# Optimization experiments

Hardware: AMD Instinct MI355X
Metric: run time of the kernel (lower is better)

The kernel has to match this reference:

```python
import jax, jax.numpy as jnp
import numpy as np

N_NEURONS = 4096
N_EDGES = 131072
N_LAYERS = 2
VOCAB = 8192
B, T = 8, 128
DECAY = 0.99


def setup_inputs() -> dict:
    key = jax.random.key(0)
    ks = jax.random.split(key, 8)
    idx = jax.random.randint(ks[0], (B, T), 0, VOCAB)
    src = jax.random.randint(ks[1], (N_EDGES,), 0, N_NEURONS)
    dst = jax.random.randint(ks[2], (N_EDGES,), 0, N_NEURONS)
    Wemb = jax.random.normal(ks[3], (VOCAB, N_NEURONS), dtype=jnp.float32) * 0.02
    Gx = jax.random.normal(ks[4], (N_EDGES,), dtype=jnp.float32) * 0.02
    Gy = jax.random.normal(ks[5], (N_EDGES,), dtype=jnp.float32) * 0.02
    Gs = jnp.ones((N_EDGES,), dtype=jnp.float32)
    W_out = jax.random.normal(ks[6], (VOCAB, N_NEURONS), dtype=jnp.float32) * 0.02
    b_out = jnp.zeros((VOCAB,), dtype=jnp.float32)
    return {"idx": idx, "src": src, "dst": dst, "Wemb": Wemb, "Gx": Gx,
            "Gy": Gy, "Gs": Gs, "W_out": W_out, "b_out": b_out}


def reference(idx, src, dst, Wemb, Gx, Gy, Gs, W_out, b_out):
    # X: [B, T, n] token embeddings
    X = Wemb[idx]
    sigma0 = jnp.zeros((src.shape[0],), dtype=Wemb.dtype)
    y0 = X[:, 0, :]  # initial y_t = embedding of first token
    Xt = jnp.transpose(X, (1, 0, 2))  # [T, B, n] for scan over time

    def step(carry, x_t):
        y_t, sigma = carry
        for _ in range(N_LAYERS):
            # A[:, d] += x_t[:, s] * sigma  (gather-mul-scatter over edges)
            A = jnp.zeros_like(x_t).at[:, dst].add(x_t[:, src] * sigma)
            # Hebbian plasticity update on edge state sigma
            hebbian = (y_t[:, src] * x_t[:, dst]).mean(0)
            sigma = (sigma + hebbian * Gs) * DECAY
            y_t = jnp.zeros_like(x_t).at[:, dst].add(jax.nn.relu(A[:, src]) * Gy)
            x_t = jax.nn.relu(jnp.zeros_like(x_t).at[:, dst].add(y_t[:, src] * Gx))
        return (y_t, sigma), x_t

    (_, sigma_final), xs = jax.lax.scan(step, (y0, sigma0), Xt)  # xs: [T, B, n]
    logits = jnp.einsum('tbn,vn->btv', xs, W_out) + b_out  # [B, T, vocab]
    return logits, sigma_final
```

## Files before the change

kernel.cpp:

```cpp
#include <hip/hip_runtime.h>
#include <cstdint>
#include <cstddef>

#define NN   4096
#define NE   131072
#define NBAT 8
#define NT   128
#define NV   8192
#define NK   4096
#define NM   1024
#define DECAYF 0.99f
#define COOP_BLOCKS 256
#define COOP_THREADS 1024
#define NBARRIERS (NT * 5)

typedef short bf16x8 __attribute__((ext_vector_type(8)));
typedef float f32x4 __attribute__((ext_vector_type(4)));
typedef unsigned short u16x8 __attribute__((ext_vector_type(8)));

__device__ __forceinline__ unsigned short f2bf(float f) {
  unsigned int u = __builtin_bit_cast(unsigned int, f);
  u = u + 0x7fffu + ((u >> 16) & 1u);
  return (unsigned short)(u >> 16);
}

__device__ __forceinline__ float cload(const float* p) {
  return __hip_atomic_load(p, __ATOMIC_RELAXED, __HIP_MEMORY_SCOPE_AGENT);
}
__device__ __forceinline__ void cstore(float* p, float v) {
  __hip_atomic_store(p, v, __ATOMIC_RELAXED, __HIP_MEMORY_SCOPE_AGENT);
}
__device__ __forceinline__ int cloadi(const int* p) {
  return __hip_atomic_load(p, __ATOMIC_RELAXED, __HIP_MEMORY_SCOPE_AGENT);
}
__device__ __forceinline__ void cstorei(int* p, int v) {
  __hip_atomic_store(p, v, __ATOMIC_RELAXED, __HIP_MEMORY_SCOPE_AGENT);
}

__global__ void k_hist(const int* __restrict__ dst, int* __restrict__ cnt) {
  int e = blockIdx.x * 256 + threadIdx.x;
  if (e < NE) atomicAdd(&cnt[dst[e]], 1);
}

__global__ void k_scan(const int* __restrict__ cnt, int* __restrict__ row_ptr,
                       int* __restrict__ cursor) {
  __shared__ int lds[256];
  int tid = threadIdx.x;
  int base = tid * 16;
  int loc[16];
  int s = 0;
  #pragma unroll
  for (int i = 0; i < 16; ++i) { loc[i] = s; s += cnt[base + i]; }
  lds[tid] = s;
  __syncthreads();
  for (int off = 1; off < 256; off <<= 1) {
    int v = lds[tid];
    int a = (tid >= off) ? lds[tid - off] : 0;
    __syncthreads();
    lds[tid] = v + a;
    __syncthreads();
  }
  int myoff = (tid == 0) ? 0 : lds[tid - 1];
  #pragma unroll
  for (int i = 0; i < 16; ++i) {
    int rp = myoff + loc[i];
    row_ptr[base + i] = rp;
    cursor[base + i] = rp;
  }
  if (tid == 255) row_ptr[NN] = lds[255];
}

__global__ void k_build(const int* __restrict__ src, const int* __restrict__ dst,
                        const float* __restrict__ Gx, const float* __restrict__ Gy,
                        const float* __restrict__ Gs, int* __restrict__ cursor,
                        int* __restrict__ src_s, int* __restrict__ orig_s,
                        float* __restrict__ Gx_s, float* __restrict__ Gy_s,
                        float* __restrict__ Gs_s) {
  int e = blockIdx.x * 256 + threadIdx.x;
  if (e >= NE) return;
  int d = dst[e];
  int pos = atomicAdd(&cursor[d], 1);
  src_s[pos] = src[e];
  orig_s[pos] = e;
  Gx_s[pos] = Gx[e];
  Gy_s[pos] = Gy[e];
  Gs_s[pos] = Gs[e];
}

__global__ void k_gatherX(const int* __restrict__ idx, const float* __restrict__ Wemb,
                          float* __restrict__ Xbuf, float* __restrict__ ybuf) {
  __shared__ float tile[256 * 9];
  int t = blockIdx.x >> 4;
  int nc = (blockIdx.x & 15) << 8;
  int tid = threadIdx.x;
  #pragma unroll
  for (int bb = 0; bb < 8; ++bb) {
    int row = idx[bb * NT + t];
    tile[tid * 9 + bb] = Wemb[(size_t)row * NN + nc + tid];
  }
  __syncthreads();
  float* dp = Xbuf + (size_t)t * (NN * NBAT) + (size_t)nc * NBAT;
  #pragma unroll
  for (int kk = 0; kk < 8; ++kk) dp[tid * 8 + kk] = tile[tid * 9 + kk];
  if (t == 0) {
    float* yp = ybuf + (size_t)nc * NBAT;
    #pragma unroll
    for (int kk = 0; kk < 8; ++kk) yp[tid * 8 + kk] = tile[tid * 9 + kk];
  }
}

__global__ void k_convW(const float* __restrict__ W, unsigned short* __restrict__ Wbf) {
  size_t base = ((size_t)blockIdx.x * 256 + threadIdx.x) * 8;
  float4 a = *(const float4*)(W + base);
  float4 b = *(const float4*)(W + base + 4);
  u16x8 hv;
  hv[0] = f2bf(a.x); hv[1] = f2bf(a.y); hv[2] = f2bf(a.z); hv[3] = f2bf(a.w);
  hv[4] = f2bf(b.x); hv[5] = f2bf(b.y); hv[6] = f2bf(b.z); hv[7] = f2bf(b.w);
  *(u16x8*)(Wbf + base) = hv;
}

__device__ __forceinline__ void gridbar(int* bar, int& gen) {
  __syncthreads();
  if (threadIdx.x == 0) {
    cstorei(&bar[blockIdx.x], gen + 1);
    while (cloadi(&bar[320]) <= gen) __builtin_amdgcn_s_sleep(1);
  }
  ++gen;
  __syncthreads();
}

__global__ __launch_bounds__(COOP_THREADS, 8) void k_loop(
    const int* __restrict__ row_ptr, const int* __restrict__ src_s,
    const float* __restrict__ Gx_s, const float* __restrict__ Gy_s,
    const float* __restrict__ Gs_s, float* __restrict__ sigma_s,
    const float* __restrict__ Xbuf, float* __restrict__ ybuf,
    float* __restrict__ xbuf, float* __restrict__ Abuf,
    unsigned short* __restrict__ Abf, int* bar,
    const int* __restrict__ orig_s, float* __restrict__ sig_out) {
  if (blockIdx.x == COOP_BLOCKS) {
    if (threadIdx.x < 64) {
      const int lane = threadIdx.x;
      for (int g = 1; g <= NBARRIERS; ++g) {
        for (;;) {
          int v0 = cloadi(&bar[lane * 4 + 0]);
          int v1 = cloadi(&bar[lane * 4 + 1]);
          int v2 = cloadi(&bar[lane * 4 + 2]);
          int v3 = cloadi(&bar[lane * 4 + 3]);
          int m = min(min(v0, v1), min(v2, v3));
          #pragma unroll
          for (int d = 1; d < 64; d <<= 1) m = min(m, __shfl_xor(m, d));
          if (m >= g) break;
        }
        if (lane == 0) cstorei(&bar[320], g);
      }
    }
    return;
  }

  const int tid = threadIdx.x;
  const int g = blockIdx.x * COOP_THREADS + tid;
  const int b = g & 7;
  const int h = (g >> 3) & 7;
  const int n = g >> 6;
  const int rs = row_ptr[n];
  const int re = row_ptr[n + 1];
  const int nb8 = (n << 3) | b;
  int gen = 0;

  for (int t = 0; t < NT; ++t) {
    const float* xp = Xbuf + (size_t)t * (NN * NBAT);
    #pragma unroll
    for (int layer = 0; layer < 2; ++layer) {
      {
        float xn = (layer == 0) ? xp[nb8] : cload(&xbuf[nb8]);
        float acc = 0.f;
        for (int j = rs + h; j < re; j += 32) {
          int jj[4], sv[4];
          float sg[4], gs[4], xv[4], yv[4];
          bool act[4];
          #pragma unroll
          for (int u = 0; u < 4; ++u) {
            int jc = j + (u << 3);
            act[u] = jc < re;
            jj[u] = act[u] ? jc : j;
          }
          #pragma unroll
          for (int u = 0; u < 4; ++u) sv[u] = src_s[jj[u]];
          #pragma unroll
          for (int u = 0; u < 4; ++u) {
            float sgu = sigma_s[jj[u]];
            float gsu = Gs_s[jj[u]];
            sg[u] = act[u] ? sgu : 0.f;
            gs[u] = act[u] ? gsu : 0.f;
          }
          #pragma unroll
          for (int u = 0; u < 4; ++u) {
            int sb = (sv[u] << 3) | b;
            xv[u] = (layer == 0) ? xp[sb] : cload(&xbuf[sb]);
            yv[u] = cload(&ybuf[sb]);
          }
          #pragma unroll
          for (int u = 0; u < 4; ++u) {
            acc = fmaf(xv[u], sg[u], acc);
            float pv = yv[u] * xn;
            pv += __shfl_xor(pv, 1);
            pv += __shfl_xor(pv, 2);
            pv += __shfl_xor(pv, 4);
            if (b == 0 && act[u])
              sigma_s[jj[u]] = (sg[u] + pv * 0.125f * gs[u]) * DECAYF;
          }
        }
        acc += __shfl_xor(acc, 8);
        acc += __shfl_xor(acc, 16);
        acc += __shfl_xor(acc, 32);
        if (h == 0) cstore(&Abuf[nb8], acc);
      }
      gridbar(bar, gen);
      {
        float acc = 0.f;
        for (int j = rs + h; j < re; j += 32) {
          int jj[4], sv[4];
          float gy[4], av[4];
          bool act[4];
          #pragma unroll
          for (int u = 0; u < 4; ++u) {
            int jc = j + (u << 3);
            act[u] = jc < re;
            jj[u] = act[u] ? jc : j;
          }
          #pragma unroll
          for (int u = 0; u < 4; ++u) sv[u] = src_s[jj[u]];
          #pragma unroll
          for (int u = 0; u < 4; ++u) {
            float gyu = Gy_s[jj[u]];
            gy[u] = act[u] ? gyu : 0.f;
          }
          #pragma unroll
          for (int u = 0; u < 4; ++u) av[u] = cload(&Abuf[(sv[u] << 3) | b]);
          #pragma unroll
          for (int u = 0; u < 4; ++u) acc = fmaf(fmaxf(av[u], 0.f), gy[u], acc);
        }
        acc += __shfl_xor(acc, 8);
        acc += __shfl_xor(acc, 16);
        acc += __shfl_xor(acc, 32);
        if (h == 0) cstore(&ybuf[nb8], acc);
      }
      gridbar(bar, gen);
      {
        float acc = 0.f;
        for (int j = rs + h; j < re; j += 32) {
          int jj[4], sv[4];
          float gx[4], yv[4];
          bool act[4];
          #pragma unroll
          for (int u = 0; u < 4; ++u) {
            int jc = j + (u << 3);
            act[u] = jc < re;
            jj[u] = act[u] ? jc : j;
          }
          #pragma unroll
          for (int u = 0; u < 4; ++u) sv[u] = src_s[jj[u]];
          #pragma unroll
          for (int u = 0; u < 4; ++u) {
            float gxu = Gx_s[jj[u]];
            gx[u] = act[u] ? gxu : 0.f;
          }
          #pragma unroll
          for (int u = 0; u < 4; ++u) yv[u] = cload(&ybuf[(sv[u] << 3) | b]);
          #pragma unroll
          for (int u = 0; u < 4; ++u) acc = fmaf(yv[u], gx[u], acc);
        }
        acc += __shfl_xor(acc, 8);
        acc += __shfl_xor(acc, 16);
        acc += __shfl_xor(acc, 32);
        if (layer == 0) {
          if (h == 0) cstore(&xbuf[nb8], fmaxf(acc, 0.f));
        } else if (h == 0) {
          Abf[(size_t)((b << 7) | t) * NK + n] = f2bf(fmaxf(acc, 0.f));
        }
      }
      if (layer == 0) {
        gridbar(bar, gen);
        xp = xbuf;
      }
    }
  }
  __syncthreads();
  int jlo = row_ptr[blockIdx.x * 16];
  int jhi = row_ptr[blockIdx.x * 16 + 16];
  for (int j = jlo + tid; j < jhi; j += COOP_THREADS) sig_out[orig_s[j]] = sigma_s[j];
}

__global__ __launch_bounds__(256) void k_gemm(const unsigned short* __restrict__ A,
                                              const unsigned short* __restrict__ Bw,
                                              const float* __restrict__ bias,
                                              float* __restrict__ C) {
  __shared__ __align__(16) unsigned short As[128 * 32];
  __shared__ __align__(16) unsigned short Bs[128 * 32];
  const int m0 = blockIdx.y * 128;
  const int v0 = blockIdx.x * 128;
  const int wave = threadIdx.x >> 6;
  const int lane = threadIdx.x & 63;
  const int wm = wave >> 1;
  const int wv = wave & 1;
  f32x4 acc[4][4] = {};

  const int srow = lane >> 2;
  const int skc = (lane & 3) * 8;

  for (int k0 = 0; k0 < NK; k0 += 32) {
    #pragma unroll
    for (int c = 0; c < 2; ++c) {
      int chunk = wave * 2 + c;
      int row = chunk * 16 + srow;
      __builtin_amdgcn_global_load_lds(
          (const __attribute__((address_space(1))) void*)(A + (size_t)(m0 + row) * NK + k0 + skc),
          (__attribute__((address_space(3))) void*)(As + chunk * 512), 16, 0, 0);
      __builtin_amdgcn_global_load_lds(
          (const __attribute__((address_space(1))) void*)(Bw + (size_t)(v0 + row) * NK + k0 + skc),
          (__attribute__((address_space(3))) void*)(Bs + chunk * 512), 16, 0, 0);
    }
    __syncthreads();
    bf16x8 af[4], bq[4];
    #pragma unroll
    for (int mi = 0; mi < 4; ++mi)
      af[mi] = *(const bf16x8*)(As + ((wm * 64 + mi * 16 + (lane & 15)) * 32 + (lane >> 4) * 8));
    #pragma unroll
    for (int ni = 0; ni < 4; ++ni)
      bq[ni] = *(const bf16x8*)(Bs + ((wv * 64 + ni * 16 + (lane & 15)) * 32 + (lane >> 4) * 8));
    #pragma unroll
    for (int mi = 0; mi < 4; ++mi)
      #pragma unroll
      for (int ni = 0; ni < 4; ++ni)
        acc[mi][ni] = __builtin_amdgcn_mfma_f32_16x16x32_bf16(af[mi], bq[ni], acc[mi][ni], 0, 0, 0);
    __syncthreads();
  }

  #pragma unroll
  for (int mi = 0; mi < 4; ++mi) {
    int mrow = m0 + wm * 64 + mi * 16 + ((lane >> 4) << 2);
    #pragma unroll
    for (int ni = 0; ni < 4; ++ni) {
      int vcol = v0 + wv * 64 + ni * 16 + (lane & 15);
      float bs = bias[vcol];
      f32x4 a = acc[mi][ni];
      #pragma unroll
      for (int r = 0; r < 4; ++r) C[(size_t)(mrow + r) * NV + vcol] = a[r] + bs;
    }
  }
}

extern "C" void kernel_launch(void* const* d_in, const int* in_sizes, int n_in,
                              void* d_out, int out_size, void* d_ws, size_t ws_size,
                              hipStream_t stream) {
  (void)in_sizes; (void)n_in; (void)out_size;
  const int*   idx  = (const int*)d_in[0];
  const int*   src  = (const int*)d_in[1];
  const int*   dst  = (const int*)d_in[2];
  const float* Wemb = (const float*)d_in[3];
  const float* Gx   = (const float*)d_in[4];
  const float* Gy   = (const float*)d_in[5];
  const float* Gs   = (const float*)d_in[6];
  const float* Wout = (const float*)d_in[7];
  const float* bout = (const float*)d_in[8];
  float* out = (float*)d_out;
  float* sig_out = out + (size_t)NM * NV;

  char* p = (char*)d_ws;
  int*   bar     = (int*)p;
  int*   cnt     = (int*)(p + 2048);
  float* sigma_s = (float*)(p + 2048 + 16384);
  size_t off = 2048 + 16384 + (size_t)NE * 4;
  const size_t msz = off;
  int*   row_ptr = (int*)(p + off); off += 16640;
  int*   cursor  = (int*)(p + off); off += 16384;
  int*   src_s   = (int*)(p + off); off += (size_t)NE * 4;
  int*   orig_s  = (int*)(p + off); off += (size_t)NE * 4;
  float* Gx_s    = (float*)(p + off); off += (size_t)NE * 4;
  float* Gy_s    = (float*)(p + off); off += (size_t)NE * 4;
  float* Gs_s    = (float*)(p + off); off += (size_t)NE * 4;
  float* ybuf    = (float*)(p + off); off += (size_t)NN * NBAT * 4;
  float* xbuf    = (float*)(p + off); off += (size_t)NN * NBAT * 4;
  float* Abuf    = (float*)(p + off); off += (size_t)NN * NBAT * 4;
  float* Xbuf    = (float*)(p + off); off += (size_t)NT * NN * NBAT * 4;
  unsigned short* Abf = (unsigned short*)(p + off); off += (size_t)NM * NK * 2;
  unsigned short* Wbf = (unsigned short*)(p + off); off += (size_t)NV * NK * 2;
  if (ws_size < off) return;

  hipMemsetAsync(d_ws, 0, msz, stream);
  k_hist<<<NE / 256, 256, 0, stream>>>(dst, cnt);
  k_scan<<<1, 256, 0, stream>>>(cnt, row_ptr, cursor);
  k_build<<<NE / 256, 256, 0, stream>>>(src, dst, Gx, Gy, Gs, cursor,
                                        src_s, orig_s, Gx_s, Gy_s, Gs_s);
  k_gatherX<<<NT * 16, 256, 0, stream>>>(idx, Wemb, Xbuf, ybuf);
  k_convW<<<(NV * NK) / (256 * 8), 256, 0, stream>>>(Wout, Wbf);
  k_loop<<<COOP_BLOCKS + 1, COOP_THREADS, 0, stream>>>(row_ptr, src_s, Gx_s, Gy_s, Gs_s,
      sigma_s, Xbuf, ybuf, xbuf, Abuf, Abf, bar, orig_s, sig_out);
  k_gemm<<<dim3(NV / 128, NM / 128), 256, 0, stream>>>(Abf, Wbf, bout, out);
}
```

Before: 3.414 ms.

## Keep per-edge sigma and source indices in registers, interleave x/y buffers

Each thread now caches its first 8 edges' source indices and sigma values in registers for the whole time loop, with a sentinel padded slot so that loads need no masking. Edges beyond 64 per destination fall back to a memory loop. x and y states are interleaved so layer-1 reads both with one 64-bit load. The grid barrier now releases through a per-block padded flag instead of one shared word, to cut contention on that word. This adds register pressure and a tail path for high in-degree nodes.

```diff
diff --git a/kernel.cpp b/kernel.cpp
--- a/kernel.cpp
+++ b/kernel.cpp
@@ -27,6 +27,11 @@
 __device__ __forceinline__ float cload(const float* p) {
   return __hip_atomic_load(p, __ATOMIC_RELAXED, __HIP_MEMORY_SCOPE_AGENT);
 }
+__device__ __forceinline__ float2 cload2(const float* p) {
+  unsigned long long v = __hip_atomic_load((const unsigned long long*)p,
+                                           __ATOMIC_RELAXED, __HIP_MEMORY_SCOPE_AGENT);
+  return __builtin_bit_cast(float2, v);
+}
 __device__ __forceinline__ void cstore(float* p, float v) {
   __hip_atomic_store(p, v, __ATOMIC_RELAXED, __HIP_MEMORY_SCOPE_AGENT);
 }
@@ -78,6 +83,10 @@
                         float* __restrict__ Gs_s) {
   int e = blockIdx.x * 256 + threadIdx.x;
   if (e >= NE) return;
+  if (e == 0) {
+    src_s[NE] = 0;
+    Gx_s[NE] = 0.f; Gy_s[NE] = 0.f; Gs_s[NE] = 0.f;
+  }
   int d = dst[e];
   int pos = atomicAdd(&cursor[d], 1);
   src_s[pos] = src[e];
@@ -88,7 +97,7 @@
 }
 
 __global__ void k_gatherX(const int* __restrict__ idx, const float* __restrict__ Wemb,
-                          float* __restrict__ Xbuf, float* __restrict__ ybuf) {
+                          float* __restrict__ Xbuf, float* __restrict__ xybuf) {
   __shared__ float tile[256 * 9];
   int t = blockIdx.x >> 4;
   int nc = (blockIdx.x & 15) << 8;
@@ -103,9 +112,9 @@
   #pragma unroll
   for (int kk = 0; kk < 8; ++kk) dp[tid * 8 + kk] = tile[tid * 9 + kk];
   if (t == 0) {
-    float* yp = ybuf + (size_t)nc * NBAT;
-    #pragma unroll
-    for (int kk = 0; kk < 8; ++kk) yp[tid * 8 + kk] = tile[tid * 9 + kk];
+    float* yp = xybuf + (size_t)nc * NBAT * 2;
+    #pragma unroll
+    for (int kk = 0; kk < 8; ++kk) yp[((tid * 8 + kk) << 1) + 1] = tile[tid * 9 + kk];
   }
 }
 
@@ -119,11 +128,11 @@
   *(u16x8*)(Wbf + base) = hv;
 }
 
-__device__ __forceinline__ void gridbar(int* bar, int& gen) {
+__device__ __forceinline__ void gridbar(int* bar, int* rel, int& gen) {
   __syncthreads();
   if (threadIdx.x == 0) {
     cstorei(&bar[blockIdx.x], gen + 1);
-    while (cloadi(&bar[320]) <= gen) __builtin_amdgcn_s_sleep(1);
+    while (cloadi(&rel[blockIdx.x << 4]) <= gen) __builtin_amdgcn_s_sleep(1);
   }
   ++gen;
   __syncthreads();
@@ -133,25 +142,26 @@
     const int* __restrict__ row_ptr, const int* __restrict__ src_s,
     const float* __restrict__ Gx_s, const float* __restrict__ Gy_s,
     const float* __restrict__ Gs_s, float* __restrict__ sigma_s,
-    const float* __restrict__ Xbuf, float* __restrict__ ybuf,
-    float* __restrict__ xbuf, float* __restrict__ Abuf,
-    unsigned short* __restrict__ Abf, int* bar,
+    const float* __restrict__ Xbuf, float* __restrict__ xybuf,
+    float* __restrict__ Abuf, unsigned short* __restrict__ Abf,
+    int* bar, int* rel,
     const int* __restrict__ orig_s, float* __restrict__ sig_out) {
   if (blockIdx.x == COOP_BLOCKS) {
     if (threadIdx.x < 64) {
       const int lane = threadIdx.x;
       for (int g = 1; g <= NBARRIERS; ++g) {
         for (;;) {
-          int v0 = cloadi(&bar[lane * 4 + 0]);
-          int v1 = cloadi(&bar[lane * 4 + 1]);
-          int v2 = cloadi(&bar[lane * 4 + 2]);
-          int v3 = cloadi(&bar[lane * 4 + 3]);
+          int v0 = cloadi(&bar[lane]);
+          int v1 = cloadi(&bar[lane + 64]);
+          int v2 = cloadi(&bar[lane + 128]);
+          int v3 = cloadi(&bar[lane + 192]);
           int m = min(min(v0, v1), min(v2, v3));
           #pragma unroll
           for (int d = 1; d < 64; d <<= 1) m = min(m, __shfl_xor(m, d));
           if (m >= g) break;
         }
-        if (lane == 0) cstorei(&bar[320], g);
+        #pragma unroll
+        for (int k = 0; k < 4; ++k) cstorei(&rel[(lane + k * 64) << 4], g);
       }
     }
     return;
@@ -164,50 +174,63 @@
   const int n = g >> 6;
   const int rs = row_ptr[n];
   const int re = row_ptr[n + 1];
+  const int rh = rs + h;
   const int nb8 = (n << 3) | b;
+  const int nb16 = nb8 << 1;
   int gen = 0;
+
+  int   r_sb[8];
+  float r_sg[8];
+  #pragma unroll
+  for (int s = 0; s < 8; ++s) {
+    int jc = rh + ((s >> 2) << 5) + ((s & 3) << 3);
+    int j = (jc < re) ? jc : NE;
+    r_sb[s] = (src_s[j] << 3) | b;
+    r_sg[s] = 0.f;
+  }
+  const bool tail = (re - rs) > 64;
 
   for (int t = 0; t < NT; ++t) {
     const float* xp = Xbuf + (size_t)t * (NN * NBAT);
     #pragma unroll
     for (int layer = 0; layer < 2; ++layer) {
       {
-        float xn = (layer == 0) ? xp[nb8] : cload(&xbuf[nb8]);
+        float xn = (layer == 0) ? xp[nb8] : cload(&xybuf[nb16]);
+        float xv[8], yv[8];
+        #pragma unroll
+        for (int s = 0; s < 8; ++s) {
+          if (layer == 0) {
+            xv[s] = xp[r_sb[s]];
+            yv[s] = cload(&xybuf[(r_sb[s] << 1) + 1]);
+          } else {
+            float2 p2 = cload2(&xybuf[r_sb[s] << 1]);
+            xv[s] = p2.x; yv[s] = p2.y;
+          }
+        }
         float acc = 0.f;
-        for (int j = rs + h; j < re; j += 32) {
-          int jj[4], sv[4];
-          float sg[4], gs[4], xv[4], yv[4];
-          bool act[4];
-          #pragma unroll
-          for (int u = 0; u < 4; ++u) {
-            int jc = j + (u << 3);
-            act[u] = jc < re;
-            jj[u] = act[u] ? jc : j;
-          }
-          #pragma unroll
-          for (int u = 0; u < 4; ++u) sv[u] = src_s[jj[u]];
-          #pragma unroll
-          for (int u = 0; u < 4; ++u) {
-            float sgu = sigma_s[jj[u]];
-            float gsu = Gs_s[jj[u]];
-            sg[u] = act[u] ? sgu : 0.f;
-            gs[u] = act[u] ? gsu : 0.f;
-          }
-          #pragma unroll
-          for (int u = 0; u < 4; ++u) {
-            int sb = (sv[u] << 3) | b;
-            xv[u] = (layer == 0) ? xp[sb] : cload(&xbuf[sb]);
-            yv[u] = cload(&ybuf[sb]);
-          }
-          #pragma unroll
-          for (int u = 0; u < 4; ++u) {
-            acc = fmaf(xv[u], sg[u], acc);
-            float pv = yv[u] * xn;
-            pv += __shfl_xor(pv, 1);
-            pv += __shfl_xor(pv, 2);
-            pv += __shfl_xor(pv, 4);
-            if (b == 0 && act[u])
-              sigma_s[jj[u]] = (sg[u] + pv * 0.125f * gs[u]) * DECAYF;
+        #pragma unroll
+        for (int s = 0; s < 8; ++s) {
+          acc = fmaf(xv[s], r_sg[s], acc);
+          float pv = yv[s] * xn;
+          pv += __shfl_xor(pv, 1);
+          pv += __shfl_xor(pv, 2);
+          pv += __shfl_xor(pv, 4);
+          int jc = rh + ((s >> 2) << 5) + ((s & 3) << 3);
+          int j = (jc < re) ? jc : NE;
+          r_sg[s] = (r_sg[s] + pv * 0.125f * Gs_s[j]) * DECAYF;
+        }
+        if (tail) {
+          for (int j = rs + 64 + h; j < re; j += 8) {
+            int sb2 = ((src_s[j] << 3) | b) << 1;
+            float xvr = (layer == 0) ? xp[sb2 >> 1] : cload(&xybuf[sb2]);
+            float yvr = cload(&xybuf[sb2 + 1]);
+            float sgr = sigma_s[j];
+            acc = fmaf(xvr, sgr, acc);
+            float pvr = yvr * xn;
+            pvr += __shfl_xor(pvr, 1);
+            pvr += __shfl_xor(pvr, 2);
+            pvr += __shfl_xor(pvr, 4);
+            if (b == 0) sigma_s[j] = (sgr + pvr * 0.125f * Gs_s[j]) * DECAYF;
           }
         }
         acc += __shfl_xor(acc, 8);
@@ -215,80 +238,62 @@
         acc += __shfl_xor(acc, 32);
         if (h == 0) cstore(&Abuf[nb8], acc);
       }
-      gridbar(bar, gen);
+      gridbar(bar, rel, gen);
       {
+        float av[8];
+        #pragma unroll
+        for (int s = 0; s < 8; ++s) av[s] = cload(&Abuf[r_sb[s]]);
         float acc = 0.f;
-        for (int j = rs + h; j < re; j += 32) {
-          int jj[4], sv[4];
-          float gy[4], av[4];
-          bool act[4];
-          #pragma unroll
-          for (int u = 0; u < 4; ++u) {
-            int jc = j + (u << 3);
-            act[u] = jc < re;
-            jj[u] = act[u] ? jc : j;
-          }
-          #pragma unroll
-          for (int u = 0; u < 4; ++u) sv[u] = src_s[jj[u]];
-          #pragma unroll
-          for (int u = 0; u < 4; ++u) {
-            float gyu = Gy_s[jj[u]];
-            gy[u] = act[u] ? gyu : 0.f;
-          }
-          #pragma unroll
-          for (int u = 0; u < 4; ++u) av[u] = cload(&Abuf[(sv[u] << 3) | b]);
-          #pragma unroll
-          for (int u = 0; u < 4; ++u) acc = fmaf(fmaxf(av[u], 0.f), gy[u], acc);
-        }
+        #pragma unroll
+        for (int s = 0; s < 8; ++s) {
+          int jc = rh + ((s >> 2) << 5) + ((s & 3) << 3);
+          int j = (jc < re) ? jc : NE;
+          acc = fmaf(fmaxf(av[s], 0.f), Gy_s[j], acc);
+        }
+        if (tail)
+          for (int j = rs + 64 + h; j < re; j += 8)
+            acc = fmaf(fmaxf(cload(&Abuf[(src_s[j] << 3) | b]), 0.f), Gy_s[j], acc);
         acc += __shfl_xor(acc, 8);
         acc += __shfl_xor(acc, 16);
         acc += __shfl_xor(acc, 32);
-        if (h == 0) cstore(&ybuf[nb8], acc);
+        if (h == 0) cstore(&xybuf[nb16 + 1], acc);
       }
-      gridbar(bar, gen);
+      gridbar(bar, rel, gen);
       {
+        float yv2[8];
+        #pragma unroll
+        for (int s = 0; s < 8; ++s) yv2[s] = cload(&xybuf[(r_sb[s] << 1) + 1]);
         float acc = 0.f;
-        for (int j = rs + h; j < re; j += 32) {
-          int jj[4], sv[4];
-          float gx[4], yv[4];
-          bool act[4];
-          #pragma unroll
-          for (int u = 0; u < 4; ++u) {
-            int jc = j + (u << 3);
-            act[u] = jc < re;
-            jj[u] = act[u] ? jc : j;
-          }
-          #pragma unroll
-          for (int u = 0; u < 4; ++u) sv[u] = src_s[jj[u]];
-          #pragma unroll
-          for (int u = 0; u < 4; ++u) {
-            float gxu = Gx_s[jj[u]];
-            gx[u] = act[u] ? gxu : 0.f;
-          }
-          #pragma unroll
-          for (int u = 0; u < 4; ++u) yv[u] = cload(&ybuf[(sv[u] << 3) | b]);
-          #pragma unroll
-          for (int u = 0; u < 4; ++u) acc = fmaf(yv[u], gx[u], acc);
-        }
+        #pragma unroll
+        for (int s = 0; s < 8; ++s) {
+          int jc = rh + ((s >> 2) << 5) + ((s & 3) << 3);
+          int j = (jc < re) ? jc : NE;
+          acc = fmaf(yv2[s], Gx_s[j], acc);
+        }
+        if (tail)
+          for (int j = rs + 64 + h; j < re; j += 8)
+            acc = fmaf(cload(&xybuf[(((src_s[j] << 3) | b) << 1) + 1]), Gx_s[j], acc);
         acc += __shfl_xor(acc, 8);
         acc += __shfl_xor(acc, 16);
         acc += __shfl_xor(acc, 32);
         if (layer == 0) {
-          if (h == 0) cstore(&xbuf[nb8], fmaxf(acc, 0.f));
+          if (h == 0) cstore(&xybuf[nb16], fmaxf(acc, 0.f));
+          gridbar(bar, rel, gen);
         } else if (h == 0) {
           Abf[(size_t)((b << 7) | t) * NK + n] = f2bf(fmaxf(acc, 0.f));
         }
       }
-      if (layer == 0) {
-        gridbar(bar, gen);
-        xp = xbuf;
-      }
     }
   }
-  __syncthreads();
-  int jlo = row_ptr[blockIdx.x * 16];
-  int jhi = row_ptr[blockIdx.x * 16 + 16];
-  for (int j = jlo + tid; j < jhi; j += COOP_THREADS) sig_out[orig_s[j]] = sigma_s[j];
+  if (b == 0) {
+    #pragma unroll
+    for (int s = 0; s < 8; ++s) {
+      int jc = rh + ((s >> 2) << 5) + ((s & 3) << 3);
+      if (jc < re) sig_out[orig_s[jc]] = r_sg[s];
+    }
+    if (tail)
+      for (int j = rs + 64 + h; j < re; j += 8) sig_out[orig_s[j]] = sigma_s[j];
+  }
 }
 
 __global__ __launch_bounds__(256) void k_gemm(const unsigned short* __restrict__ A,
@@ -368,19 +373,19 @@
 
   char* p = (char*)d_ws;
   int*   bar     = (int*)p;
-  int*   cnt     = (int*)(p + 2048);
-  float* sigma_s = (float*)(p + 2048 + 16384);
-  size_t off = 2048 + 16384 + (size_t)NE * 4;
+  int*   rel     = (int*)(p + 1024);
+  int*   cnt     = (int*)(p + 1024 + 16384);
+  float* sigma_s = (float*)(p + 1024 + 16384 + 16384);
+  size_t off = 1024 + 16384 + 16384 + (size_t)NE * 4;
   const size_t msz = off;
   int*   row_ptr = (int*)(p + off); off += 16640;
   int*   cursor  = (int*)(p + off); off += 16384;
-  int*   src_s   = (int*)(p + off); off += (size_t)NE * 4;
-  int*   orig_s  = (int*)(p + off); off += (size_t)NE * 4;
-  float* Gx_s    = (float*)(p + off); off += (size_t)NE * 4;
-  float* Gy_s    = (float*)(p + off); off += (size_t)NE * 4;
-  float* Gs_s    = (float*)(p + off); off += (size_t)NE * 4;
-  float* ybuf    = (float*)(p + off); off += (size_t)NN * NBAT * 4;
-  float* xbuf    = (float*)(p + off); off += (size_t)NN * NBAT * 4;
+  int*   src_s   = (int*)(p + off); off += (size_t)NE * 4 + 16;
+  int*   orig_s  = (int*)(p + off); off += (size_t)NE * 4 + 16;
+  float* Gx_s    = (float*)(p + off); off += (size_t)NE * 4 + 16;
+  float* Gy_s    = (float*)(p + off); off += (size_t)NE * 4 + 16;
+  float* Gs_s    = (float*)(p + off); off += (size_t)NE * 4 + 16;
+  float* xybuf   = (float*)(p + off); off += (size_t)NN * NBAT * 8;
   float* Abuf    = (float*)(p + off); off += (size_t)NN * NBAT * 4;
   float* Xbuf    = (float*)(p + off); off += (size_t)NT * NN * NBAT * 4;
   unsigned short* Abf = (unsigned short*)(p + off); off += (size_t)NM * NK * 2;
@@ -392,9 +397,9 @@
   k_scan<<<1, 256, 0, stream>>>(cnt, row_ptr, cursor);
   k_build<<<NE / 256, 256, 0, stream>>>(src, dst, Gx, Gy, Gs, cursor,
                                         src_s, orig_s, Gx_s, Gy_s, Gs_s);
-  k_gatherX<<<NT * 16, 256, 0, stream>>>(idx, Wemb, Xbuf, ybuf);
+  k_gatherX<<<NT * 16, 256, 0, stream>>>(idx, Wemb, Xbuf, xybuf);
   k_convW<<<(NV * NK) / (256 * 8), 256, 0, stream>>>(Wout, Wbf);
   k_loop<<<COOP_BLOCKS + 1, COOP_THREADS, 0, stream>>>(row_ptr, src_s, Gx_s, Gy_s, Gs_s,
-      sigma_s, Xbuf, ybuf, xbuf, Abuf, Abf, bar, orig_s, sig_out);
+      sigma_s, Xbuf, xybuf, Abuf, Abf, bar, rel, orig_s, sig_out);
   k_gemm<<<dim3(NV / 128, NM / 128), 256, 0, stream>>>(Abf, Wbf, bout, out);
 }
```

New measurement: 5.676 ms. 1.66x slower.
